# Kernel tuning notes

Hardware: AMD Instinct MI355X
Metric: run time of the kernel (lower is better)

The kernel has to match this reference:

```python
import jax, jax.numpy as jnp
import numpy as np

B, S, D, H = 2, 2048, 1024, 16
DK = D // H  # 64
SQRT_DK = DK ** 0.5
NEG = -1e9


def setup_inputs() -> dict:
    key = jax.random.key(0)
    ks = jax.random.split(key, 7)
    scale = 1.0 / np.sqrt(D)
    return {
        "x": jax.random.normal(ks[0], (B, S, D), jnp.float32),
        "encoder_output": jax.random.normal(ks[1], (B, S, D), jnp.float32),
        "mask": jax.random.randint(ks[2], (B, S), 0, 2, jnp.int32),
        "WQ": jax.random.normal(ks[3], (D, D), jnp.float32) * scale,
        "WK": jax.random.normal(ks[4], (D, D), jnp.float32) * scale,
        "WV": jax.random.normal(ks[5], (D, D), jnp.float32) * scale,
        "WO": jax.random.normal(ks[6], (D, D), jnp.float32) * scale,
    }


def reference(x, encoder_output, mask, WQ, WK, WV, WO):
    b, s, d = x.shape
    # project and split heads: (b, h, s, dk)
    q = (x @ WQ).reshape(b, s, H, DK).transpose(0, 2, 1, 3)
    k = (encoder_output @ WK).reshape(b, s, H, DK).transpose(0, 2, 1, 3)
    v = (encoder_output @ WV).reshape(b, s, H, DK).transpose(0, 2, 1, 3)
    # scores: (b, h, s_q, s_k)
    scores = jnp.einsum('bhqd,bhkd->bhqk', q, k) / SQRT_DK
    # future mask (strict upper triangle) + padding mask broadcast over key dim
    future = jnp.triu(jnp.ones((s, s), jnp.int32), 1)  # (s, s)
    m = mask[:, None, :, None] + future[None, None, :, :]  # (b, 1->h, s_q, s_k)
    scores = jnp.where(m != 0, NEG, scores)
    attn = jax.nn.softmax(scores, axis=-1)
    # context: (b, s, h, dk) -> (b, s, d)
    ctx = jnp.einsum('bhqk,bhkd->bqhd', attn, v).reshape(b, s, d)
    return ctx @ WO
```

## Files before the change

kernel.cpp:

```cpp
#include <hip/hip_runtime.h>
#include <hip/hip_bf16.h>

constexpr int B = 2, S = 2048, D = 1024, H = 16, DK = 64;
constexpr int M = B * S;
constexpr float LOG2E = 1.44269504088896f;
constexpr float NEGBIG = -3.0e38f;
constexpr float QSCALE = 0.125f * LOG2E;

using short8 = __attribute__((ext_vector_type(8))) short;
using short4v = __attribute__((ext_vector_type(4))) short;
using f32x4 = __attribute__((ext_vector_type(4))) float;

#define GLOBAL_AS __attribute__((address_space(1)))
#define LDS_AS __attribute__((address_space(3)))

__device__ __forceinline__ void gll16(const void* g, void* l) {
  __builtin_amdgcn_global_load_lds((const GLOBAL_AS void*)g, (LDS_AS void*)l, 16, 0, 0);
}

__device__ __forceinline__ short f2bf(float f) {
  __hip_bfloat16 h = __float2bfloat16(f);
  short s;
  __builtin_memcpy(&s, &h, 2);
  return s;
}
__device__ __forceinline__ float bf2f(short s) {
  __hip_bfloat16 h;
  __builtin_memcpy(&h, &s, 2);
  return __bfloat162float(h);
}
__device__ __forceinline__ unsigned pack2bf(float a, float b) {
  return (unsigned)(unsigned short)f2bf(a) | ((unsigned)(unsigned short)f2bf(b) << 16);
}

__global__ __launch_bounds__(256) void prep_kernel(const float* __restrict__ x,
                                                   const float* __restrict__ enc,
                                                   const float* __restrict__ W0,
                                                   const float* __restrict__ W1,
                                                   const float* __restrict__ W2,
                                                   const float* __restrict__ W3,
                                                   short* __restrict__ xb,
                                                   short* __restrict__ encb,
                                                   short* __restrict__ Wt) {
  __shared__ float t[64][65];
  const int bx = blockIdx.x;
  if (bx < 8192) {
    const float4* src = (const float4*)((bx & 4096) ? enc : x);
    short4v* dst = (short4v*)((bx & 4096) ? encb : xb);
    const int i = (bx & 4095) * 256 + threadIdx.x;
    const float4 v = src[i];
    short4v o;
    o[0] = f2bf(v.x); o[1] = f2bf(v.y); o[2] = f2bf(v.z); o[3] = f2bf(v.w);
    dst[i] = o;
  } else {
    const int idx = bx - 8192;
    const int z = idx >> 8, rem = idx & 255;
    const float* W = z == 0 ? W0 : z == 1 ? W1 : z == 2 ? W2 : W3;
    short* dstw = Wt + (size_t)z * D * D;
    const int n0 = (rem & 15) * 64, k0 = (rem >> 4) * 64;
    const int lx = threadIdx.x & 63, ly = threadIdx.x >> 6;
    #pragma unroll
    for (int r = 0; r < 64; r += 4)
      t[r + ly][lx] = W[(size_t)(k0 + r + ly) * D + n0 + lx];
    __syncthreads();
    #pragma unroll
    for (int r = 0; r < 64; r += 4)
      dstw[(size_t)(n0 + r + ly) * D + k0 + lx] = f2bf(t[lx][r + ly]);
  }
}

__global__ __launch_bounds__(256) void gemm_qkv_kernel(const short* __restrict__ A0,
                                                       const short* __restrict__ A1,
                                                       const short* __restrict__ Wts,
                                                       short* __restrict__ Cv,
                                                       float* __restrict__ vsum) {
  __shared__ short As[2][4][128][8];
  __shared__ short Bs[2][4][128][8];
  const int z = blockIdx.z;
  const short* __restrict__ A = z ? A1 : A0;
  const short* __restrict__ Bt = Wts + (size_t)z * D * D;
  const float oscale = (z == 0) ? QSCALE : 1.0f;

  const int tid = threadIdx.x;
  const int lane = tid & 63, wid = tid >> 6;
  const int l15 = lane & 15, lg = lane >> 4;
  const int row0 = blockIdx.y * 128, col0 = blockIdx.x * 128;
  const int wm = wid >> 1, wn = wid & 1;
  f32x4 acc[4][4] = {};

  auto stage = [&](int k0, int nb) {
    #pragma unroll
    for (int it = 0; it < 2; ++it) {
      const int c = tid + it * 256;
      const int row = c & 127, kc2 = c >> 7;
      gll16(&A[(size_t)(row0 + row) * D + k0 + kc2 * 8],
            (char*)As + nb * 8192 + (wid * 64 + it * 256) * 16);
      gll16(&Bt[(size_t)(col0 + row) * D + k0 + kc2 * 8],
            (char*)Bs + nb * 8192 + (wid * 64 + it * 256) * 16);
    }
  };

  stage(0, 0);
  __syncthreads();
  int cur = 0;
  for (int t = 0; t < D / 32; ++t) {
    if (t < D / 32 - 1) stage((t + 1) * 32, cur ^ 1);
    short8 af[4], bfr[4];
    #pragma unroll
    for (int m = 0; m < 4; ++m) af[m] = *(const short8*)&As[cur][lg][wm * 64 + m * 16 + l15][0];
    #pragma unroll
    for (int n = 0; n < 4; ++n) bfr[n] = *(const short8*)&Bs[cur][lg][wn * 64 + n * 16 + l15][0];
    #pragma unroll
    for (int m = 0; m < 4; ++m)
      #pragma unroll
      for (int n = 0; n < 4; ++n)
        acc[m][n] = __builtin_amdgcn_mfma_f32_16x16x32_bf16(af[m], bfr[n], acc[m][n], 0, 0, 0);
    __syncthreads();
    cur ^= 1;
  }
  #pragma unroll
  for (int m = 0; m < 4; ++m) {
    #pragma unroll
    for (int r = 0; r < 4; ++r) {
      const int row = row0 + wm * 64 + m * 16 + 4 * lg + r;
      #pragma unroll
      for (int n = 0; n < 4; ++n) {
        const int col = col0 + wn * 64 + n * 16 + l15;
        Cv[(size_t)z * M * D + (size_t)row * D + col] = f2bf(acc[m][n][r] * oscale);
      }
    }
  }
  if (z == 2) {
    const int bidx = row0 >> 11;
    #pragma unroll
    for (int n = 0; n < 4; ++n) {
      float s = 0.f;
      #pragma unroll
      for (int m = 0; m < 4; ++m)
        s += acc[m][n][0] + acc[m][n][1] + acc[m][n][2] + acc[m][n][3];
      s += __shfl_xor(s, 16);
      s += __shfl_xor(s, 32);
      if (lg == 0) atomicAdd(&vsum[(size_t)bidx * D + col0 + wn * 64 + n * 16 + l15], s);
    }
  }
}

__global__ __launch_bounds__(256) void gemmO_kernel(const short* __restrict__ A,
                                                    const short* __restrict__ Bt,
                                                    float* __restrict__ C) {
  __shared__ short As[2][4][128][8];
  __shared__ short Bs[2][4][64][8];
  const int tid = threadIdx.x;
  const int lane = tid & 63, wid = tid >> 6;
  const int l15 = lane & 15, lg = lane >> 4;
  const int col0 = blockIdx.x * 64, row0 = blockIdx.y * 128;
  const int wm = wid >> 1, wn = wid & 1;
  f32x4 acc[4][2] = {};

  auto stage = [&](int k0, int nb) {
    #pragma unroll
    for (int it = 0; it < 2; ++it) {
      const int c = tid + it * 256;
      const int row = c & 127, kc2 = c >> 7;
      gll16(&A[(size_t)(row0 + row) * D + k0 + kc2 * 8],
            (char*)As + nb * 8192 + (wid * 64 + it * 256) * 16);
    }
    gll16(&Bt[(size_t)(col0 + lane) * D + k0 + wid * 8],
          (char*)Bs + nb * 4096 + wid * 1024);
  };

  stage(0, 0);
  __syncthreads();
  int cur = 0;
  for (int t = 0; t < D / 32; ++t) {
    if (t < D / 32 - 1) stage((t + 1) * 32, cur ^ 1);
    short8 af[4], bfr[2];
    #pragma unroll
    for (int m = 0; m < 4; ++m) af[m] = *(const short8*)&As[cur][lg][wm * 64 + m * 16 + l15][0];
    #pragma unroll
    for (int n = 0; n < 2; ++n) bfr[n] = *(const short8*)&Bs[cur][lg][wn * 32 + n * 16 + l15][0];
    #pragma unroll
    for (int m = 0; m < 4; ++m)
      #pragma unroll
      for (int n = 0; n < 2; ++n)
        acc[m][n] = __builtin_amdgcn_mfma_f32_16x16x32_bf16(af[m], bfr[n], acc[m][n], 0, 0, 0);
    __syncthreads();
    cur ^= 1;
  }
  #pragma unroll
  for (int m = 0; m < 4; ++m)
    #pragma unroll
    for (int r = 0; r < 4; ++r) {
      const int row = row0 + wm * 64 + m * 16 + 4 * lg + r;
      #pragma unroll
      for (int n = 0; n < 2; ++n)
        C[(size_t)row * D + col0 + wn * 32 + n * 16 + l15] = acc[m][n][r];
    }
}

__device__ __forceinline__ int keyof(int c, int i) {
  return ((c >> 1) << 5) + ((i >> 2) << 3) + ((c & 1) << 2) + (i & 3);
}
__device__ __forceinline__ int vt_byte(int kc, int d, int ksb) {
  return kc * 1024 + ((d ^ (kc & 7)) << 4) + ksb * 2;
}

__global__ __launch_bounds__(512, 4) void attn_kernel(const short* __restrict__ Qb,
                                                      const short* __restrict__ Kb,
                                                      const short* __restrict__ Vb,
                                                      const int* __restrict__ maskp,
                                                      const float* __restrict__ vsum,
                                                      short* __restrict__ ctxb) {
  __shared__ short KsBuf[2][4096];
  __shared__ short VtBuf[2][4096];
  const int h = blockIdx.x, iblk = blockIdx.y, b = blockIdx.z;
  const int qtA = iblk, qtB = 31 - iblk;
  const int tid = threadIdx.x, lane = tid & 63, wid = tid >> 6;
  const int grp = wid >> 2, wq = wid & 3;
  const int qt = grp ? qtB : qtA;
  const int l15 = lane & 15, lg = lane >> 4;

  short8 qf[2];
  {
    const size_t o = (size_t)(b * S + qt * 64 + wq * 16 + l15) * D + h * DK;
    qf[0] = *(const short8*)&Qb[o + lg * 8];
    qf[1] = *(const short8*)&Qb[o + 32 + lg * 8];
  }
  float m = NEGBIG, l = 0.f;
  f32x4 cx[4] = {};

  const int kkey = keyof(lg, l15);
  const int vu = tid & 31, dv = tid >> 5;
  const int vkc = vu >> 2, vksb = (vu & 3) * 2;

  auto stageK = [&](int j, int nb) {
    gll16(&Kb[(size_t)(b * S + j * 64 + kkey) * D + h * DK + wid * 8],
          (char*)KsBuf + nb * 8192 + wid * 1024);
  };
  auto loadV = [&](int j, short4v& va, short4v& vb2) {
    const size_t vb0 = (size_t)(b * S + j * 64 + 2 * vu) * D + h * DK + dv * 4;
    va = *(const short4v*)&Vb[vb0];
    vb2 = *(const short4v*)&Vb[vb0 + D];
  };
  auto writeV = [&](int nb, const short4v& va, const short4v& vb2) {
    #pragma unroll
    for (int i = 0; i < 4; ++i) {
      const unsigned w = (unsigned)(unsigned short)va[i] | ((unsigned)(unsigned short)vb2[i] << 16);
      *(unsigned*)((char*)VtBuf + nb * 8192 + vt_byte(vkc, dv * 4 + i, vksb)) = w;
    }
  };

  auto tile = [&](bool diag, int nb) {
    const char* ksb_ = (const char*)KsBuf + nb * 8192;
    const char* vtb_ = (const char*)VtBuf + nb * 8192;
    f32x4 sa[4];
    __builtin_amdgcn_s_setprio(1);
    #pragma unroll
    for (int c = 0; c < 4; ++c) {
      const short8 kf0 = *(const short8*)(ksb_ + lg * 1024 + c * 256 + l15 * 16);
      const short8 kf1 = *(const short8*)(ksb_ + (4 + lg) * 1024 + c * 256 + l15 * 16);
      f32x4 zz = {0.f, 0.f, 0.f, 0.f};
      zz = __builtin_amdgcn_mfma_f32_16x16x32_bf16(kf0, qf[0], zz, 0, 0, 0);
      zz = __builtin_amdgcn_mfma_f32_16x16x32_bf16(kf1, qf[1], zz, 0, 0, 0);
      sa[c] = zz;
    }
    __builtin_amdgcn_s_setprio(0);
    if (diag) {
      const int ql = wq * 16 + l15;
      #pragma unroll
      for (int c = 0; c < 4; ++c)
        #pragma unroll
        for (int r = 0; r < 4; ++r)
          if (((c >> 1) << 5) + (lg << 3) + ((c & 1) << 2) + r > ql) sa[c][r] = NEGBIG;
    }
    float pm = sa[0][0];
    #pragma unroll
    for (int c = 0; c < 4; ++c)
      #pragma unroll
      for (int r = 0; r < 4; ++r) pm = fmaxf(pm, sa[c][r]);
    pm = fmaxf(pm, __shfl_xor(pm, 16));
    pm = fmaxf(pm, __shfl_xor(pm, 32));
    if (pm > m + 8.f) {
      const float sc = exp2f(m - pm);
      l *= sc;
      #pragma unroll
      for (int dt = 0; dt < 4; ++dt) cx[dt] *= sc;
      m = pm;
    }
    float rs = 0.f;
    #pragma unroll
    for (int c = 0; c < 4; ++c)
      #pragma unroll
      for (int r = 0; r < 4; ++r) {
        const float p = exp2f(sa[c][r] - m);
        sa[c][r] = p;
        rs += p;
      }
    rs += __shfl_xor(rs, 16);
    rs += __shfl_xor(rs, 32);
    l += rs;
    short8 pf[2];
    #pragma unroll
    for (int kk = 0; kk < 2; ++kk)
      #pragma unroll
      for (int jj = 0; jj < 8; ++jj)
        pf[kk][jj] = f2bf(sa[kk * 2 + (jj >> 2)][jj & 3]);
    __builtin_amdgcn_s_setprio(1);
    #pragma unroll
    for (int kk = 0; kk < 2; ++kk)
      #pragma unroll
      for (int dt = 0; dt < 4; ++dt) {
        const short8 vf = *(const short8*)(vtb_ + vt_byte(kk * 4 + lg, dt * 16 + l15, 0));
        cx[dt] = __builtin_amdgcn_mfma_f32_16x16x32_bf16(vf, pf[kk], cx[dt], 0, 0, 0);
      }
    __builtin_amdgcn_s_setprio(0);
  };

  {
    short4v va, vb2;
    stageK(0, 0);
    loadV(0, va, vb2);
    writeV(0, va, vb2);
  }
  __syncthreads();
  int cur = 0;
  for (int j = 0; j <= qtB; ++j) {
    short4v nva, nvb;
    if (j < qtB) { stageK(j + 1, cur ^ 1); loadV(j + 1, nva, nvb); }
    if (j <= qt) tile(j == qt, cur);
    if (j < qtB) writeV(cur ^ 1, nva, nvb);
    __syncthreads();
    cur ^= 1;
  }

  {
    const int qg = qt * 64 + wq * 16 + l15;
    const int mq = maskp[b * S + qg];
    const float inv = 1.0f / l;
    constexpr float vscale = 1.0f / S;
    short* orow = &ctxb[(size_t)(b * S + qg) * D + h * DK];
    const float* vmb = &vsum[(size_t)b * D + h * DK];
    #pragma unroll
    for (int dt = 0; dt < 4; ++dt)
      #pragma unroll
      for (int p2 = 0; p2 < 2; ++p2) {
        const int d = dt * 16 + 4 * lg + p2 * 2;
        const float v0 = mq ? vmb[d] * vscale     : cx[dt][p2 * 2] * inv;
        const float v1 = mq ? vmb[d + 1] * vscale : cx[dt][p2 * 2 + 1] * inv;
        *(unsigned*)&orow[d] = pack2bf(v0, v1);
      }
  }
}

extern "C" void kernel_launch(void* const* d_in, const int* in_sizes, int n_in,
                              void* d_out, int out_size, void* d_ws, size_t ws_size,
                              hipStream_t stream) {
  (void)in_sizes; (void)n_in; (void)out_size; (void)ws_size;
  const float* x   = (const float*)d_in[0];
  const float* enc = (const float*)d_in[1];
  const int*   msk = (const int*)d_in[2];
  const float* WQ  = (const float*)d_in[3];
  const float* WK  = (const float*)d_in[4];
  const float* WV  = (const float*)d_in[5];
  const float* WO  = (const float*)d_in[6];
  float* out = (float*)d_out;

  char* ws = (char*)d_ws;
  const size_t MB = 1u << 20;
  short* xb    = (short*)(ws + 0);
  short* encb  = (short*)(ws + 8 * MB);
  short* Qb    = (short*)(ws + 16 * MB);
  short* WQt   = (short*)(ws + 40 * MB);
  float* vsum  = (float*)(ws + 48 * MB);
  short* Kb    = Qb + (size_t)M * D;
  short* Vb    = Kb + (size_t)M * D;
  short* WOt   = WQt + (size_t)3 * D * D;
  short* ctxb  = xb;

  hipMemsetAsync(vsum, 0, (size_t)B * D * sizeof(float), stream);

  prep_kernel<<<dim3(9216), 256, 0, stream>>>(x, enc, WQ, WK, WV, WO, xb, encb, WQt);

  gemm_qkv_kernel<<<dim3(D / 128, M / 128, 3), 256, 0, stream>>>(xb, encb, WQt, Qb, vsum);

  attn_kernel<<<dim3(H, 16, B), 512, 0, stream>>>(Qb, Kb, Vb, msk, vsum, ctxb);

  gemmO_kernel<<<dim3(D / 64, M / 128), 256, 0, stream>>>(ctxb, WOt, out);
}
```

Measured before the change: 183.0 us.

## Process 128-key chunks per attention barrier and swap GEMM grid axes

The attention kernel now stages two 64-key tiles (128 keys) of K and transposed V per iteration and handles them with a single max/rescale pass. This halves the number of block-wide barriers and amortises the online-softmax bookkeeping, and V loads are widened to 16-byte vectors. The price is twice the LDS use (64 KB per block), which may lower occupancy, plus some padding work at the causal boundary. The QKV and output GEMMs also swap grid x/y so that consecutive blocks walk along rows, which changes L2 reuse of the weight tiles; the setprio hints are removed.

```diff
diff --git a/kernel.cpp b/kernel.cpp
--- a/kernel.cpp
+++ b/kernel.cpp
@@ -23,11 +23,6 @@
   short s;
   __builtin_memcpy(&s, &h, 2);
   return s;
-}
-__device__ __forceinline__ float bf2f(short s) {
-  __hip_bfloat16 h;
-  __builtin_memcpy(&h, &s, 2);
-  return __bfloat162float(h);
 }
 __device__ __forceinline__ unsigned pack2bf(float a, float b) {
   return (unsigned)(unsigned short)f2bf(a) | ((unsigned)(unsigned short)f2bf(b) << 16);
@@ -84,7 +79,7 @@
   const int tid = threadIdx.x;
   const int lane = tid & 63, wid = tid >> 6;
   const int l15 = lane & 15, lg = lane >> 4;
-  const int row0 = blockIdx.y * 128, col0 = blockIdx.x * 128;
+  const int row0 = blockIdx.x * 128, col0 = blockIdx.y * 128;
   const int wm = wid >> 1, wn = wid & 1;
   f32x4 acc[4][4] = {};
 
@@ -153,7 +148,7 @@
   const int tid = threadIdx.x;
   const int lane = tid & 63, wid = tid >> 6;
   const int l15 = lane & 15, lg = lane >> 4;
-  const int col0 = blockIdx.x * 64, row0 = blockIdx.y * 128;
+  const int row0 = blockIdx.x * 128, col0 = blockIdx.y * 64;
   const int wm = wid >> 1, wn = wid & 1;
   f32x4 acc[4][2] = {};
 
@@ -211,8 +206,8 @@
                                                       const int* __restrict__ maskp,
                                                       const float* __restrict__ vsum,
                                                       short* __restrict__ ctxb) {
-  __shared__ short KsBuf[2][4096];
-  __shared__ short VtBuf[2][4096];
+  __shared__ char KsBuf[2][16384];
+  __shared__ char VtBuf[2][16384];
   const int h = blockIdx.x, iblk = blockIdx.y, b = blockIdx.z;
   const int qtA = iblk, qtB = 31 - iblk;
   const int tid = threadIdx.x, lane = tid & 63, wid = tid >> 6;
@@ -230,54 +225,80 @@
   f32x4 cx[4] = {};
 
   const int kkey = keyof(lg, l15);
-  const int vu = tid & 31, dv = tid >> 5;
-  const int vkc = vu >> 2, vksb = (vu & 3) * 2;
-
-  auto stageK = [&](int j, int nb) {
-    gll16(&Kb[(size_t)(b * S + j * 64 + kkey) * D + h * DK + wid * 8],
-          (char*)KsBuf + nb * 8192 + wid * 1024);
-  };
-  auto loadV = [&](int j, short4v& va, short4v& vb2) {
-    const size_t vb0 = (size_t)(b * S + j * 64 + 2 * vu) * D + h * DK + dv * 4;
-    va = *(const short4v*)&Vb[vb0];
-    vb2 = *(const short4v*)&Vb[vb0 + D];
-  };
-  auto writeV = [&](int nb, const short4v& va, const short4v& vb2) {
-    #pragma unroll
-    for (int i = 0; i < 4; ++i) {
+  const int vu = tid & 63, dv = tid >> 6;
+  const int vh = vu >> 5, vl = vu & 31;
+  const int vkc = vl >> 2, vksb = (vl & 3) * 2;
+
+  auto stageK = [&](int jc, int nb) {
+    const size_t base = (size_t)(b * S + jc * 128 + kkey) * D + h * DK + wid * 8;
+    gll16(&Kb[base], (char*)KsBuf + nb * 16384 + wid * 1024);
+    gll16(&Kb[base + (size_t)64 * D], (char*)KsBuf + nb * 16384 + 8192 + wid * 1024);
+  };
+  auto loadV = [&](int jc, short8& va, short8& vb2) {
+    const size_t vb0 = (size_t)(b * S + jc * 128 + 2 * vu) * D + h * DK + dv * 8;
+    va = *(const short8*)&Vb[vb0];
+    vb2 = *(const short8*)&Vb[vb0 + D];
+  };
+  auto writeV = [&](int nb, const short8& va, const short8& vb2) {
+    char* dst = (char*)VtBuf + nb * 16384 + vh * 8192;
+    #pragma unroll
+    for (int i = 0; i < 8; ++i) {
       const unsigned w = (unsigned)(unsigned short)va[i] | ((unsigned)(unsigned short)vb2[i] << 16);
-      *(unsigned*)((char*)VtBuf + nb * 8192 + vt_byte(vkc, dv * 4 + i, vksb)) = w;
-    }
-  };
-
-  auto tile = [&](bool diag, int nb) {
-    const char* ksb_ = (const char*)KsBuf + nb * 8192;
-    const char* vtb_ = (const char*)VtBuf + nb * 8192;
-    f32x4 sa[4];
-    __builtin_amdgcn_s_setprio(1);
+      *(unsigned*)(dst + vt_byte(vkc, dv * 8 + i, vksb)) = w;
+    }
+  };
+
+  auto tile_pair = [&](int nb, bool do1, bool diag0, bool diag1) {
+    const char* ks0 = (const char*)KsBuf + nb * 16384;
+    const char* ks1 = ks0 + 8192;
+    const char* vt0 = (const char*)VtBuf + nb * 16384;
+    const char* vt1 = vt0 + 8192;
+    f32x4 sa0[4], sa1[4];
     #pragma unroll
     for (int c = 0; c < 4; ++c) {
-      const short8 kf0 = *(const short8*)(ksb_ + lg * 1024 + c * 256 + l15 * 16);
-      const short8 kf1 = *(const short8*)(ksb_ + (4 + lg) * 1024 + c * 256 + l15 * 16);
+      const short8 kf0 = *(const short8*)(ks0 + lg * 1024 + c * 256 + l15 * 16);
+      const short8 kf1 = *(const short8*)(ks0 + (4 + lg) * 1024 + c * 256 + l15 * 16);
       f32x4 zz = {0.f, 0.f, 0.f, 0.f};
       zz = __builtin_amdgcn_mfma_f32_16x16x32_bf16(kf0, qf[0], zz, 0, 0, 0);
       zz = __builtin_amdgcn_mfma_f32_16x16x32_bf16(kf1, qf[1], zz, 0, 0, 0);
-      sa[c] = zz;
-    }
-    __builtin_amdgcn_s_setprio(0);
-    if (diag) {
-      const int ql = wq * 16 + l15;
+      sa0[c] = zz;
+    }
+    if (do1) {
+      #pragma unroll
+      for (int c = 0; c < 4; ++c) {
+        const short8 kf0 = *(const short8*)(ks1 + lg * 1024 + c * 256 + l15 * 16);
+        const short8 kf1 = *(const short8*)(ks1 + (4 + lg) * 1024 + c * 256 + l15 * 16);
+        f32x4 zz = {0.f, 0.f, 0.f, 0.f};
+        zz = __builtin_amdgcn_mfma_f32_16x16x32_bf16(kf0, qf[0], zz, 0, 0, 0);
+        zz = __builtin_amdgcn_mfma_f32_16x16x32_bf16(kf1, qf[1], zz, 0, 0, 0);
+        sa1[c] = zz;
+      }
+    }
+    const int ql = wq * 16 + l15;
+    if (diag0) {
       #pragma unroll
       for (int c = 0; c < 4; ++c)
         #pragma unroll
         for (int r = 0; r < 4; ++r)
-          if (((c >> 1) << 5) + (lg << 3) + ((c & 1) << 2) + r > ql) sa[c][r] = NEGBIG;
-    }
-    float pm = sa[0][0];
+          if (((c >> 1) << 5) + (lg << 3) + ((c & 1) << 2) + r > ql) sa0[c][r] = NEGBIG;
+    }
+    if (do1 && diag1) {
+      #pragma unroll
+      for (int c = 0; c < 4; ++c)
+        #pragma unroll
+        for (int r = 0; r < 4; ++r)
+          if (((c >> 1) << 5) + (lg << 3) + ((c & 1) << 2) + r > ql) sa1[c][r] = NEGBIG;
+    }
+    float pm = sa0[0][0];
     #pragma unroll
     for (int c = 0; c < 4; ++c)
       #pragma unroll
-      for (int r = 0; r < 4; ++r) pm = fmaxf(pm, sa[c][r]);
+      for (int r = 0; r < 4; ++r) pm = fmaxf(pm, sa0[c][r]);
+    if (do1)
+      #pragma unroll
+      for (int c = 0; c < 4; ++c)
+        #pragma unroll
+        for (int r = 0; r < 4; ++r) pm = fmaxf(pm, sa1[c][r]);
     pm = fmaxf(pm, __shfl_xor(pm, 16));
     pm = fmaxf(pm, __shfl_xor(pm, 32));
     if (pm > m + 8.f) {
@@ -292,43 +313,69 @@
     for (int c = 0; c < 4; ++c)
       #pragma unroll
       for (int r = 0; r < 4; ++r) {
-        const float p = exp2f(sa[c][r] - m);
-        sa[c][r] = p;
+        const float p = exp2f(sa0[c][r] - m);
+        sa0[c][r] = p;
         rs += p;
       }
+    if (do1)
+      #pragma unroll
+      for (int c = 0; c < 4; ++c)
+        #pragma unroll
+        for (int r = 0; r < 4; ++r) {
+          const float p = exp2f(sa1[c][r] - m);
+          sa1[c][r] = p;
+          rs += p;
+        }
     rs += __shfl_xor(rs, 16);
     rs += __shfl_xor(rs, 32);
     l += rs;
-    short8 pf[2];
-    #pragma unroll
-    for (int kk = 0; kk < 2; ++kk)
-      #pragma unroll
-      for (int jj = 0; jj < 8; ++jj)
-        pf[kk][jj] = f2bf(sa[kk * 2 + (jj >> 2)][jj & 3]);
-    __builtin_amdgcn_s_setprio(1);
-    #pragma unroll
-    for (int kk = 0; kk < 2; ++kk)
-      #pragma unroll
-      for (int dt = 0; dt < 4; ++dt) {
-        const short8 vf = *(const short8*)(vtb_ + vt_byte(kk * 4 + lg, dt * 16 + l15, 0));
-        cx[dt] = __builtin_amdgcn_mfma_f32_16x16x32_bf16(vf, pf[kk], cx[dt], 0, 0, 0);
-      }
-    __builtin_amdgcn_s_setprio(0);
-  };
-
+    {
+      short8 pf[2];
+      #pragma unroll
+      for (int kk = 0; kk < 2; ++kk)
+        #pragma unroll
+        for (int jj = 0; jj < 8; ++jj)
+          pf[kk][jj] = f2bf(sa0[kk * 2 + (jj >> 2)][jj & 3]);
+      #pragma unroll
+      for (int kk = 0; kk < 2; ++kk)
+        #pragma unroll
+        for (int dt = 0; dt < 4; ++dt) {
+          const short8 vf = *(const short8*)(vt0 + vt_byte(kk * 4 + lg, dt * 16 + l15, 0));
+          cx[dt] = __builtin_amdgcn_mfma_f32_16x16x32_bf16(vf, pf[kk], cx[dt], 0, 0, 0);
+        }
+    }
+    if (do1) {
+      short8 pf[2];
+      #pragma unroll
+      for (int kk = 0; kk < 2; ++kk)
+        #pragma unroll
+        for (int jj = 0; jj < 8; ++jj)
+          pf[kk][jj] = f2bf(sa1[kk * 2 + (jj >> 2)][jj & 3]);
+      #pragma unroll
+      for (int kk = 0; kk < 2; ++kk)
+        #pragma unroll
+        for (int dt = 0; dt < 4; ++dt) {
+          const short8 vf = *(const short8*)(vt1 + vt_byte(kk * 4 + lg, dt * 16 + l15, 0));
+          cx[dt] = __builtin_amdgcn_mfma_f32_16x16x32_bf16(vf, pf[kk], cx[dt], 0, 0, 0);
+        }
+    }
+  };
+
+  const int nB = (qtB >> 1) + 1;
   {
-    short4v va, vb2;
+    short8 va, vb2;
     stageK(0, 0);
     loadV(0, va, vb2);
     writeV(0, va, vb2);
   }
   __syncthreads();
   int cur = 0;
-  for (int j = 0; j <= qtB; ++j) {
-    short4v nva, nvb;
-    if (j < qtB) { stageK(j + 1, cur ^ 1); loadV(j + 1, nva, nvb); }
-    if (j <= qt) tile(j == qt, cur);
-    if (j < qtB) writeV(cur ^ 1, nva, nvb);
+  for (int jc = 0; jc < nB; ++jc) {
+    short8 nva, nvb;
+    if (jc + 1 < nB) { stageK(jc + 1, cur ^ 1); loadV(jc + 1, nva, nvb); }
+    const int t0 = 2 * jc, t1 = 2 * jc + 1;
+    if (t0 <= qt) tile_pair(cur, t1 <= qt, t0 == qt, t1 == qt);
+    if (jc + 1 < nB) writeV(cur ^ 1, nva, nvb);
     __syncthreads();
     cur ^= 1;
   }
@@ -381,9 +428,9 @@
 
   prep_kernel<<<dim3(9216), 256, 0, stream>>>(x, enc, WQ, WK, WV, WO, xb, encb, WQt);
 
-  gemm_qkv_kernel<<<dim3(D / 128, M / 128, 3), 256, 0, stream>>>(xb, encb, WQt, Qb, vsum);
+  gemm_qkv_kernel<<<dim3(M / 128, D / 128, 3), 256, 0, stream>>>(xb, encb, WQt, Qb, vsum);
 
   attn_kernel<<<dim3(H, 16, B), 512, 0, stream>>>(Qb, Kb, Vb, msk, vsum, ctxb);
 
-  gemmO_kernel<<<dim3(D / 64, M / 128), 256, 0, stream>>>(ctxb, WOt, out);
-}
+  gemmO_kernel<<<dim3(M / 128, D / 64), 256, 0, stream>>>(ctxb, WOt, out);
+}
```

Measured after the change: 167.5 us. -8.5%, faster.
